# Kernel tuning notes

Measured on AMD Instinct MI355X. Metric: run time of the kernel, lower is better.

The kernel has to match this reference:

```python
import jax, jax.numpy as jnp
import numpy as np

MARGIN = 50.0

def setup_inputs() -> dict:
    key = jax.random.key(0)
    k1, k2 = jax.random.split(key)
    N, D = 4096, 768
    rep_anchor = jax.random.normal(k1, (N, D), dtype=jnp.float32)
    rep_pos = jax.random.normal(k2, (N, D), dtype=jnp.float32)
    return {"rep_anchor": rep_anchor, "rep_pos": rep_pos}

def reference(rep_anchor, rep_pos):
    # pairwise euclidean distances: dist[i, j] = ||anchor_i - pos_j||_2
    # (F.pairwise_distance with p=2, eps handled implicitly; use stable sqrt)
    a2 = jnp.sum(rep_anchor * rep_anchor, axis=1, keepdims=True)   # [N,1]
    p2 = jnp.sum(rep_pos * rep_pos, axis=1, keepdims=True).T       # [1,N]
    cross = rep_anchor @ rep_pos.T                                  # [N,N]
    sq = jnp.maximum(a2 + p2 - 2.0 * cross, 0.0)
    dist = jnp.sqrt(sq + 1e-12)
    scores = MARGIN - dist                                          # [N,N]
    # row-wise negative log-softmax, take diagonal (positive pair at index i)
    logp = jax.nn.log_softmax(scores, axis=1)
    loss_per_row = -jnp.diagonal(logp)                               # [N]
    return loss_per_row.mean()
```

## Files before the change

### kernel.cpp

```cpp
#include <hip/hip_runtime.h>
#include <hip/hip_bf16.h>
#include <hip/hip_fp8.h>
#include <stdint.h>


#define N_ROWS 4096
#define D_DIM  768
#define NITER (D_DIM / 64)
#define ABUF  (256 * 64)
#define BBUF  (128 * 64)

typedef float f32x4 __attribute__((ext_vector_type(4)));
typedef int   i32x4 __attribute__((ext_vector_type(4)));

__global__ __launch_bounds__(256) void cvt_norms(
        const float* __restrict__ A, const float* __restrict__ P,
        uint8_t* __restrict__ A8, uint8_t* __restrict__ P8,
        float* __restrict__ a2, float* __restrict__ p2, float* __restrict__ S) {
    const int t = threadIdx.x, lane = t & 63, wave = t >> 6;
    const int row = blockIdx.x * 4 + wave;
    const float* src = blockIdx.y ? P : A;
    uint8_t* dst = blockIdx.y ? P8 : A8;
    float* nrm = blockIdx.y ? p2 : a2;

    const float4* s4 = (const float4*)src + (size_t)row * (D_DIM / 4);
    uint32_t* d4 = (uint32_t*)dst + (size_t)row * (D_DIM / 4);
    float s = 0.0f;
#pragma unroll
    for (int c = 0; c < 3; c++) {
        const int wf = c * 64 + lane;
        float4 v = s4[wf];
        s += v.x * v.x + v.y * v.y + v.z * v.z + v.w * v.w;
        union { uint32_t u; uint8_t b[4]; } pk;
        pk.b[0] = __hip_fp8_e4m3(v.x).__x;
        pk.b[1] = __hip_fp8_e4m3(v.y).__x;
        pk.b[2] = __hip_fp8_e4m3(v.z).__x;
        pk.b[3] = __hip_fp8_e4m3(v.w).__x;
        const int kb = wf >> 4, w16 = wf & 15;
        const int gw = w16 >> 1, h = w16 & 1;
        const int gp = ((gw & 3) << 1) | (gw >> 2);
        d4[(kb << 4) + (gp << 1) + h] = pk.u;
    }
    for (int off = 32; off; off >>= 1) s += __shfl_down(s, off);
    if (lane == 0) {
        nrm[row] = s;
        if (blockIdx.y == 0) S[row] = 0.0f;
    }
}

__device__ __forceinline__ void g2l16(const void* g, void* l) {
    __builtin_amdgcn_global_load_lds(
        (const __attribute__((address_space(1))) void*)g,
        (__attribute__((address_space(3))) void*)l, 16, 0, 0);
}

__global__ __launch_bounds__(512, 4) void gemm_fused(
        const uint8_t* __restrict__ A8, const uint8_t* __restrict__ P8,
        const float* __restrict__ a2, const float* __restrict__ p2,
        float* __restrict__ S, float* __restrict__ Dd) {
    __shared__ __align__(16) uint8_t As[3 * ABUF];
    __shared__ __align__(16) uint8_t Bs[3 * BBUF];

    const int lin = blockIdx.x;
    const int swz = (lin & 7) * 64 + (lin >> 3);
    const int bm = swz & 15, bn = swz >> 4;

    const int t = threadIdx.x;
    const int lane = t & 63, wave = t >> 6;
    const int wm = wave >> 1, wn = wave & 1;

    f32x4 acc[4][4];
#pragma unroll
    for (int i = 0; i < 4; i++)
#pragma unroll
        for (int j = 0; j < 4; j++) acc[i][j] = (f32x4){0.f, 0.f, 0.f, 0.f};

    const int gT = ((t & 3) - (t >> 3)) & 3;
    const size_t aBase = (size_t)(bm * 256 + (t >> 2)) * D_DIM + (size_t)gT * 16;
    const size_t bBase = (size_t)(bn * 128 + (t >> 2)) * D_DIM + (size_t)gT * 16;

    const int fr = lane & 15, fq = lane >> 4;
    int aOff[4], bOff[4];
#pragma unroll
    for (int mi = 0; mi < 4; mi++) {
        const int R = wm * 64 + mi * 16 + fr;
        aOff[mi] = R * 64 + ((fq + (R >> 1)) & 3) * 16;
    }
#pragma unroll
    for (int ni = 0; ni < 4; ni++) {
        const int R = wn * 64 + ni * 16 + fr;
        bOff[ni] = R * 64 + ((fq + (R >> 1)) & 3) * 16;
    }

#define STAGE(K2, SEL)                                                            \
    do {                                                                          \
        const int k0_ = (K2) * 64;                                                \
        _Pragma("unroll")                                                         \
        for (int c = 0; c < 2; c++)                                               \
            g2l16(A8 + aBase + (size_t)c * (128 * D_DIM) + k0_,                   \
                  &As[(SEL) * ABUF + (c * 512 + t) * 16]);                        \
        g2l16(P8 + bBase + k0_, &Bs[(SEL) * BBUF + t * 16]);                      \
    } while (0)

    STAGE(0, 0);
    STAGE(1, 1);

    int s0 = 0;
    for (int k = 0; k < NITER; k++) {
        if (k == NITER - 1) asm volatile("s_waitcnt vmcnt(0)" ::: "memory");
        else                asm volatile("s_waitcnt vmcnt(3)" ::: "memory");
        asm volatile("s_barrier" ::: "memory");
        if (k + 2 < NITER) {
            int s2 = s0 + 2; if (s2 >= 3) s2 -= 3;
            STAGE(k + 2, s2);
        }

        const int lbA = s0 * ABUF, lbB = s0 * BBUF;
        i32x4 av[4], bv[4];
#pragma unroll
        for (int mi = 0; mi < 4; mi++)
            av[mi] = *(const i32x4*)&As[lbA + aOff[mi]];
#pragma unroll
        for (int ni = 0; ni < 4; ni++)
            bv[ni] = *(const i32x4*)&Bs[lbB + bOff[ni]];
#pragma unroll
        for (int step = 0; step < 2; step++) {
#pragma unroll
            for (int mi = 0; mi < 4; mi++) {
                const long long afh = ((const long long*)&av[mi])[step];
#pragma unroll
                for (int ni = 0; ni < 4; ni++) {
                    const long long bfh = ((const long long*)&bv[ni])[step];
                    acc[mi][ni] = __builtin_amdgcn_mfma_f32_16x16x32_fp8_fp8(
                        afh, bfh, acc[mi][ni], 0, 0, 0);
                }
            }
        }
        s0 = (s0 == 2) ? 0 : s0 + 1;
    }
#undef STAGE

    float p2v[4];
#pragma unroll
    for (int ni = 0; ni < 4; ni++)
        p2v[ni] = p2[bn * 128 + wn * 64 + ni * 16 + fr];
    const int colBase = bn * 128 + wn * 64 + fr;

#pragma unroll
    for (int mi = 0; mi < 4; mi++) {
#pragma unroll
        for (int r = 0; r < 4; r++) {
            const int gi = bm * 256 + wm * 64 + mi * 16 + fq * 4 + r;
            const float a2v = a2[gi];
            float rs = 0.0f;
#pragma unroll
            for (int ni = 0; ni < 4; ni++) {
                const float cross = acc[mi][ni][r];
                const float sq = a2v + p2v[ni] - 2.0f * cross;
                const float dist = sqrtf(fmaxf(sq, 0.0f) + 1e-12f);
                const int gj = colBase + ni * 16;
                if (gi == gj) Dd[gi] = dist;
                rs += __expf(-dist);
            }
            rs += __shfl_xor(rs, 1);
            rs += __shfl_xor(rs, 2);
            rs += __shfl_xor(rs, 4);
            rs += __shfl_xor(rs, 8);
            if (fr == 0) atomicAdd(&S[gi], rs);
        }
    }
}

__global__ __launch_bounds__(1024) void finalize(
        const float* __restrict__ S, const float* __restrict__ Dd,
        float* __restrict__ out) {
    const int t = threadIdx.x;
    float s = 0.0f;
    for (int i = t; i < N_ROWS; i += 1024) s += Dd[i] + logf(S[i]);
    for (int off = 32; off; off >>= 1) s += __shfl_down(s, off);
    __shared__ float wsum[16];
    if ((t & 63) == 0) wsum[t >> 6] = s;
    __syncthreads();
    if (t == 0) {
        float acc = 0.0f;
#pragma unroll
        for (int w = 0; w < 16; w++) acc += wsum[w];
        out[0] = acc * (1.0f / N_ROWS);
    }
}

__global__ void zero_out1(float* __restrict__ out) {
    if (threadIdx.x == 0 && blockIdx.x == 0) out[0] = 0.0f;
}
__global__ void naive_row(const float* __restrict__ A, const float* __restrict__ P,
                          float* __restrict__ out) {
    __shared__ float arow[D_DIM];
    const int i = blockIdx.x, t = threadIdx.x;
    for (int c = t; c < D_DIM; c += 256) arow[c] = A[(size_t)i * D_DIM + c];
    __syncthreads();
    float sumexp = 0.0f, ddiag = 0.0f;
    for (int j = t; j < N_ROWS; j += 256) {
        const float* p = P + (size_t)j * D_DIM;
        float d2 = 0.0f;
        for (int c = 0; c < D_DIM; c++) { float df = arow[c] - p[c]; d2 += df * df; }
        float dist = sqrtf(fmaxf(d2, 0.0f) + 1e-12f);
        if (j == i) ddiag = dist;
        sumexp += __expf(-dist);
    }
    for (int off = 32; off; off >>= 1) {
        sumexp += __shfl_down(sumexp, off);
        ddiag  += __shfl_down(ddiag, off);
    }
    __shared__ float w1[4], w2[4];
    if ((t & 63) == 0) { w1[t >> 6] = sumexp; w2[t >> 6] = ddiag; }
    __syncthreads();
    if (t == 0) {
        float se = w1[0] + w1[1] + w1[2] + w1[3];
        float dd = w2[0] + w2[1] + w2[2] + w2[3];
        atomicAdd(out, (dd + logf(se)) * (1.0f / N_ROWS));
    }
}

extern "C" void kernel_launch(void* const* d_in, const int* in_sizes, int n_in,
                              void* d_out, int out_size, void* d_ws, size_t ws_size,
                              hipStream_t stream) {
    const float* A = (const float*)d_in[0];
    const float* P = (const float*)d_in[1];
    float* out = (float*)d_out;

    const size_t F8_BYTES = (size_t)N_ROWS * D_DIM;
    const size_t V_BYTES  = (size_t)N_ROWS * sizeof(float);
    const size_t NEED = 2 * F8_BYTES + 4 * V_BYTES;

    if (ws_size >= NEED) {
        char* ws = (char*)d_ws;
        uint8_t* A8 = (uint8_t*)(ws);
        uint8_t* P8 = (uint8_t*)(ws + F8_BYTES);
        float* a2 = (float*)(ws + 2 * F8_BYTES);
        float* p2 = (float*)(ws + 2 * F8_BYTES + V_BYTES);
        float* S  = (float*)(ws + 2 * F8_BYTES + 2 * V_BYTES);
        float* Dd = (float*)(ws + 2 * F8_BYTES + 3 * V_BYTES);

        hipLaunchKernelGGL(cvt_norms, dim3(N_ROWS / 4, 2), dim3(256), 0, stream,
                           A, P, A8, P8, a2, p2, S);
        hipLaunchKernelGGL(gemm_fused, dim3(512), dim3(512), 0, stream,
                           A8, P8, a2, p2, S, Dd);
        hipLaunchKernelGGL(finalize, dim3(1), dim3(1024), 0, stream, S, Dd, out);
    } else {
        hipLaunchKernelGGL(zero_out1, dim3(1), dim3(64), 0, stream, out);
        hipLaunchKernelGGL(naive_row, dim3(N_ROWS), dim3(256), 0, stream, A, P, out);
    }
}
```

Before: 101.7 us.

## Split the GEMM tile across 16 waves with 1024-thread blocks

Doubles the gemm_fused block to 1024 threads. Each wave now computes a 32x64 sub-tile instead of 64x64 within the same 256x128 block tile. Each thread issues a single A global-to-LDS load per stage, B loads are limited to the first 512 threads, and the vmcnt waits are adjusted per wave group. The aim is more waves in flight to hide memory and MFMA latency with fewer accumulator registers per thread, at the cost of more redundant B-fragment LDS reads and heavier barrier synchronisation across 16 waves.

Result: slower. 106.0 us (+4.3%).

```diff
diff --git a/kernel.cpp b/kernel.cpp
--- a/kernel.cpp
+++ b/kernel.cpp
@@ -54,7 +54,7 @@
         (__attribute__((address_space(3))) void*)l, 16, 0, 0);
 }
 
-__global__ __launch_bounds__(512, 4) void gemm_fused(
+__global__ __launch_bounds__(1024, 8) void gemm_fused(
         const uint8_t* __restrict__ A8, const uint8_t* __restrict__ P8,
         const float* __restrict__ a2, const float* __restrict__ p2,
         float* __restrict__ S, float* __restrict__ Dd) {
@@ -69,9 +69,9 @@
     const int lane = t & 63, wave = t >> 6;
     const int wm = wave >> 1, wn = wave & 1;
 
-    f32x4 acc[4][4];
-#pragma unroll
-    for (int i = 0; i < 4; i++)
+    f32x4 acc[2][4];
+#pragma unroll
+    for (int i = 0; i < 2; i++)
 #pragma unroll
         for (int j = 0; j < 4; j++) acc[i][j] = (f32x4){0.f, 0.f, 0.f, 0.f};
 
@@ -80,26 +80,16 @@
     const size_t bBase = (size_t)(bn * 128 + (t >> 2)) * D_DIM + (size_t)gT * 16;
 
     const int fr = lane & 15, fq = lane >> 4;
-    int aOff[4], bOff[4];
-#pragma unroll
-    for (int mi = 0; mi < 4; mi++) {
-        const int R = wm * 64 + mi * 16 + fr;
-        aOff[mi] = R * 64 + ((fq + (R >> 1)) & 3) * 16;
-    }
-#pragma unroll
-    for (int ni = 0; ni < 4; ni++) {
-        const int R = wn * 64 + ni * 16 + fr;
-        bOff[ni] = R * 64 + ((fq + (R >> 1)) & 3) * 16;
-    }
+    const int Ra = wm * 32 + fr;
+    const int aOff0 = Ra * 64 + ((fq + (Ra >> 1)) & 3) * 16;
+    const int Rb = wn * 64 + fr;
+    const int bOff0 = Rb * 64 + ((fq + (Rb >> 1)) & 3) * 16;
 
 #define STAGE(K2, SEL)                                                            \
     do {                                                                          \
         const int k0_ = (K2) * 64;                                                \
-        _Pragma("unroll")                                                         \
-        for (int c = 0; c < 2; c++)                                               \
-            g2l16(A8 + aBase + (size_t)c * (128 * D_DIM) + k0_,                   \
-                  &As[(SEL) * ABUF + (c * 512 + t) * 16]);                        \
-        g2l16(P8 + bBase + k0_, &Bs[(SEL) * BBUF + t * 16]);                      \
+        g2l16(A8 + aBase + k0_, &As[(SEL) * ABUF + t * 16]);                      \
+        if (t < 512) g2l16(P8 + bBase + k0_, &Bs[(SEL) * BBUF + t * 16]);         \
     } while (0)
 
     STAGE(0, 0);
@@ -107,8 +97,9 @@
 
     int s0 = 0;
     for (int k = 0; k < NITER; k++) {
-        if (k == NITER - 1) asm volatile("s_waitcnt vmcnt(0)" ::: "memory");
-        else                asm volatile("s_waitcnt vmcnt(3)" ::: "memory");
+        if (k == NITER - 1)  asm volatile("s_waitcnt vmcnt(0)" ::: "memory");
+        else if (wave < 8)   asm volatile("s_waitcnt vmcnt(2)" ::: "memory");
+        else                 asm volatile("s_waitcnt vmcnt(1)" ::: "memory");
         asm volatile("s_barrier" ::: "memory");
         if (k + 2 < NITER) {
             int s2 = s0 + 2; if (s2 >= 3) s2 -= 3;
@@ -116,18 +107,16 @@
         }
 
         const int lbA = s0 * ABUF, lbB = s0 * BBUF;
-        i32x4 av[4], bv[4];
-#pragma unroll
-        for (int mi = 0; mi < 4; mi++)
-            av[mi] = *(const i32x4*)&As[lbA + aOff[mi]];
+        i32x4 bv[4];
 #pragma unroll
         for (int ni = 0; ni < 4; ni++)
-            bv[ni] = *(const i32x4*)&Bs[lbB + bOff[ni]];
-#pragma unroll
-        for (int step = 0; step < 2; step++) {
-#pragma unroll
-            for (int mi = 0; mi < 4; mi++) {
-                const long long afh = ((const long long*)&av[mi])[step];
+            bv[ni] = *(const i32x4*)&Bs[lbB + bOff0 + ni * 1024];
+#pragma unroll
+        for (int mi = 0; mi < 2; mi++) {
+            const i32x4 av = *(const i32x4*)&As[lbA + aOff0 + mi * 1024];
+#pragma unroll
+            for (int step = 0; step < 2; step++) {
+                const long long afh = ((const long long*)&av)[step];
 #pragma unroll
                 for (int ni = 0; ni < 4; ni++) {
                     const long long bfh = ((const long long*)&bv[ni])[step];
@@ -147,10 +136,10 @@
     const int colBase = bn * 128 + wn * 64 + fr;
 
 #pragma unroll
-    for (int mi = 0; mi < 4; mi++) {
+    for (int mi = 0; mi < 2; mi++) {
 #pragma unroll
         for (int r = 0; r < 4; r++) {
-            const int gi = bm * 256 + wm * 64 + mi * 16 + fq * 4 + r;
+            const int gi = bm * 256 + wm * 32 + mi * 16 + fq * 4 + r;
             const float a2v = a2[gi];
             float rs = 0.0f;
 #pragma unroll
@@ -243,7 +232,7 @@
 
         hipLaunchKernelGGL(cvt_norms, dim3(N_ROWS / 4, 2), dim3(256), 0, stream,
                            A, P, A8, P8, a2, p2, S);
-        hipLaunchKernelGGL(gemm_fused, dim3(512), dim3(512), 0, stream,
+        hipLaunchKernelGGL(gemm_fused, dim3(512), dim3(1024), 0, stream,
                            A8, P8, a2, p2, S, Dd);
         hipLaunchKernelGGL(finalize, dim3(1), dim3(1024), 0, stream, S, Dd, out);
     } else {
```
